# Optimization experiments

Measured on AMD Instinct MI355X. Metric: run time of the kernel, lower is better.

Reference implementation:

```python
import jax, jax.numpy as jnp
import numpy as np

EPS = 1e-8  # torch cosine_similarity default eps


def setup_inputs() -> dict:
    key = jax.random.key(0)
    x = jax.random.normal(key, (256, 200, 1024), dtype=jnp.float32)
    return {"x": x}


def reference(x):
    # x: [B, c, l]
    # Cosine-similarity Gram matrix, fused: dot(i,j) / max(||x_i||*||x_j||, eps)
    norms = jnp.linalg.norm(x, axis=-1)                      # [B, c]
    dots = jnp.einsum('bil,bjl->bij', x, x)                  # [B, c, c]
    sim = dots / jnp.maximum(norms[:, :, None] * norms[:, None, :], EPS)
    atten = jax.nn.softmax(sim, axis=-1)                     # [B, c, c]
    out = jnp.einsum('bij,bjl->bil', atten, x) + x           # bmm + residual
    return out
```

## Files before the change

### kernel.cpp

```cpp
#include <hip/hip_runtime.h>
#include <math.h>


typedef unsigned int uint32;
typedef __attribute__((ext_vector_type(8))) short bf16x8;
typedef __attribute__((ext_vector_type(4))) float f32x4;

#define CC 200
#define LL 1024
#define EPSV 1e-8f
#define PLSTR 116
#define XASTR 36
#define TSTR 116

__device__ __forceinline__ uint32 bfb(float f) {
  uint32 u = __float_as_uint(f);
  u += 0x7fffu + ((u >> 16) & 1u);
  return u >> 16;
}

__global__ __launch_bounds__(512, 1)
void spe_attn_kernel(const float* __restrict__ x, float* __restrict__ out) {
  const int tid  = threadIdx.x;
  const int lane = tid & 63;
  const int w    = tid >> 6;
  const int lm   = lane & 15;
  const int lg   = lane >> 4;
  const int bidx = blockIdx.x;
  const float* xb = x + (size_t)bidx * (CC * LL);
  float* ob       = out + (size_t)bidx * (CC * LL);

  __shared__ uint32 LDS[39312];
  uint32* pl    = LDS;
  uint32* xa0   = LDS + 24128;
  uint32* xa1   = LDS + 31616;
  uint32* xbf0  = LDS + 24128;
  uint32* xbf1  = LDS + 31616;
  float*  norms = (float*)(LDS + 39104);

  const bool two = (w < 5);
  const int rb0 = w;
  const int rb1 = two ? (w + 8) : w;

  const f32x4 fz = {0.f, 0.f, 0.f, 0.f};
  f32x4 acc[2][13];
  #pragma unroll
  for (int i = 0; i < 2; ++i)
    #pragma unroll
    for (int j = 0; j < 13; ++j) acc[i][j] = fz;

  if (tid < 288) { xa0[7200 + tid] = 0u; xa1[7200 + tid] = 0u; }

  float4 vst[7];
  #pragma unroll
  for (int i = 0; i < 7; ++i) {
    int idx = tid + i * 512;
    if (idx < 3200) {
      int row = idx >> 4, c4 = idx & 15;
      vst[i] = *(const float4*)(xb + row * LL + c4 * 4);
    }
  }
  #pragma unroll
  for (int i = 0; i < 7; ++i) {
    int idx = tid + i * 512;
    if (idx < 3200) {
      int row = idx >> 4, c4 = idx & 15;
      uint2 wv;
      wv.x = bfb(vst[i].x) | (bfb(vst[i].y) << 16);
      wv.y = bfb(vst[i].z) | (bfb(vst[i].w) << 16);
      *(uint2*)&xa0[row * XASTR + c4 * 2] = wv;
    }
  }

  for (int s = 0; s < 16; ++s) {
    __syncthreads();
    if (s + 1 < 16) {
      #pragma unroll
      for (int i = 0; i < 7; ++i) {
        int idx = tid + i * 512;
        if (idx < 3200) {
          int row = idx >> 4, c4 = idx & 15;
          vst[i] = *(const float4*)(xb + row * LL + (s + 1) * 64 + c4 * 4);
        }
      }
    }
    const uint32* cur = (s & 1) ? xa1 : xa0;
    __builtin_amdgcn_s_setprio(1);
    #pragma unroll
    for (int ks = 0; ks < 2; ++ks) {
      bf16x8 a0 = *(const bf16x8*)&cur[(rb0 * 16 + lm) * XASTR + ks * 16 + lg * 4];
      bf16x8 a1 = a0;
      if (two) a1 = *(const bf16x8*)&cur[(rb1 * 16 + lm) * XASTR + ks * 16 + lg * 4];
      #pragma unroll
      for (int ct = 0; ct < 13; ++ct) {
        bf16x8 bf = *(const bf16x8*)&cur[(ct * 16 + lm) * XASTR + ks * 16 + lg * 4];
        acc[0][ct] = __builtin_amdgcn_mfma_f32_16x16x32_bf16(a0, bf, acc[0][ct], 0, 0, 0);
        if (two)
          acc[1][ct] = __builtin_amdgcn_mfma_f32_16x16x32_bf16(a1, bf, acc[1][ct], 0, 0, 0);
      }
    }
    __builtin_amdgcn_s_setprio(0);
    if (s + 1 < 16) {
      uint32* nxt = (s & 1) ? xa0 : xa1;
      #pragma unroll
      for (int i = 0; i < 7; ++i) {
        int idx = tid + i * 512;
        if (idx < 3200) {
          int row = idx >> 4, c4 = idx & 15;
          uint2 wv;
          wv.x = bfb(vst[i].x) | (bfb(vst[i].y) << 16);
          wv.y = bfb(vst[i].z) | (bfb(vst[i].w) << 16);
          *(uint2*)&nxt[row * XASTR + c4 * 2] = wv;
        }
      }
    }
  }

  #pragma unroll
  for (int rbi = 0; rbi < 2; ++rbi) {
    if (rbi == 0 || two) {
      int rb = rbi ? rb1 : rb0;
      #pragma unroll
      for (int ct = 0; ct < 13; ++ct) {
        if (ct == rb) {
          #pragma unroll
          for (int r = 0; r < 4; ++r) {
            int ri = lg * 4 + r;
            if (lm == ri) norms[rb * 16 + ri] = sqrtf(acc[rbi][ct][r]);
          }
        }
      }
    }
  }
  __syncthreads();

  float cn[13];
  #pragma unroll
  for (int ct = 0; ct < 13; ++ct) cn[ct] = norms[ct * 16 + lm];

  #pragma unroll
  for (int rbi = 0; rbi < 2; ++rbi) {
    if (rbi == 0 || two) {
      int rb = rbi ? rb1 : rb0;
      #pragma unroll
      for (int r = 0; r < 4; ++r) {
        int grow = rb * 16 + lg * 4 + r;
        float rn = norms[grow];
        float sv[13];
        float m = -INFINITY;
        #pragma unroll
        for (int ct = 0; ct < 13; ++ct) {
          int gc = ct * 16 + lm;
          float sval = acc[rbi][ct][r] / fmaxf(rn * cn[ct], EPSV);
          sval = (gc < CC) ? sval : -INFINITY;
          sv[ct] = sval;
          m = fmaxf(m, sval);
        }
        #pragma unroll
        for (int off = 1; off < 16; off <<= 1) m = fmaxf(m, __shfl_xor(m, off));
        float sum = 0.f;
        #pragma unroll
        for (int ct = 0; ct < 13; ++ct) {
          float e = __expf(sv[ct] - m);
          sv[ct] = e;
          sum += e;
        }
        #pragma unroll
        for (int off = 1; off < 16; off <<= 1) sum += __shfl_xor(sum, off);
        float inv = 1.0f / sum;
        #pragma unroll
        for (int ct = 0; ct < 13; ++ct) {
          int gc = ct * 16 + lm;
          float p = sv[ct] * inv + ((gc == grow) ? 1.0f : 0.0f);
          uint32 pb = bfb(p);
          uint32 qb = (uint32)__shfl_xor((int)pb, 1);
          if (!(lane & 1)) pl[grow * PLSTR + ct * 8 + (lm >> 1)] = pb | (qb << 16);
        }
      }
      for (int i = lane; i < 256; i += 64) {
        int rr = i >> 4, c = i & 15;
        if (c < 12) pl[(rb * 16 + rr) * PLSTR + 100 + c] = 0u;
      }
    }
  }

  bf16x8 pa[2][7];
  #pragma unroll
  for (int ks = 0; ks < 7; ++ks) {
    pa[0][ks] = *(const bf16x8*)&pl[(rb0 * 16 + lm) * PLSTR + ks * 16 + lg * 4];
    if (two)
      pa[1][ks] = *(const bf16x8*)&pl[(rb1 * 16 + lm) * PLSTR + ks * 16 + lg * 4];
  }

  float pv[7][4];
  const int swz = ((lane >> 3) & 3) << 1;
  #pragma unroll
  for (int p = 0; p < 7; ++p) {
    int rb4 = (p * 8 + w) * 4;
    #pragma unroll
    for (int q = 0; q < 4; ++q) {
      int r = rb4 + q;
      pv[p][q] = (r < CC) ? xb[r * LL + lane] : 0.f;
    }
  }
  #pragma unroll
  for (int p = 0; p < 7; ++p) {
    int kpp = p * 8 + w;
    uint2 wv;
    wv.x = bfb(pv[p][0]) | (bfb(pv[p][1]) << 16);
    wv.y = bfb(pv[p][2]) | (bfb(pv[p][3]) << 16);
    *(uint2*)&xbf0[lane * TSTR + 2 * (kpp ^ swz)] = wv;
  }

  for (int nc = 0; nc < 16; ++nc) {
    const int n0 = nc * 64;
    __syncthreads();
    if (nc + 1 < 16) {
      const int n1 = n0 + 64;
      #pragma unroll
      for (int p = 0; p < 7; ++p) {
        int rb4 = (p * 8 + w) * 4;
        #pragma unroll
        for (int q = 0; q < 4; ++q) {
          int r = rb4 + q;
          pv[p][q] = (r < CC) ? xb[r * LL + n1 + lane] : 0.f;
        }
      }
    }

    const uint32* XC = (nc & 1) ? xbf1 : xbf0;
    f32x4 acc2[2][4];
    #pragma unroll
    for (int i = 0; i < 2; ++i)
      #pragma unroll
      for (int j = 0; j < 4; ++j) acc2[i][j] = fz;

    __builtin_amdgcn_s_setprio(1);
    #pragma unroll
    for (int ks = 0; ks < 7; ++ks) {
      #pragma unroll
      for (int ct = 0; ct < 4; ++ct) {
        int col = ct * 16 + lm;
        int s2 = ((col >> 3) & 3) << 1;
        bf16x8 b = *(const bf16x8*)&XC[col * TSTR + 2 * ((ks * 8 + lg * 2) ^ s2)];
        acc2[0][ct] = __builtin_amdgcn_mfma_f32_16x16x32_bf16(pa[0][ks], b, acc2[0][ct], 0, 0, 0);
        if (two)
          acc2[1][ct] = __builtin_amdgcn_mfma_f32_16x16x32_bf16(pa[1][ks], b, acc2[1][ct], 0, 0, 0);
      }
    }
    __builtin_amdgcn_s_setprio(0);

    if (nc + 1 < 16) {
      uint32* XN = (nc & 1) ? xbf0 : xbf1;
      #pragma unroll
      for (int p = 0; p < 7; ++p) {
        int kpp = p * 8 + w;
        uint2 wv;
        wv.x = bfb(pv[p][0]) | (bfb(pv[p][1]) << 16);
        wv.y = bfb(pv[p][2]) | (bfb(pv[p][3]) << 16);
        *(uint2*)&XN[lane * TSTR + 2 * (kpp ^ swz)] = wv;
      }
    }

    #pragma unroll
    for (int rbi = 0; rbi < 2; ++rbi) {
      if (rbi == 0 || two) {
        int rb = rbi ? rb1 : rb0;
        #pragma unroll
        for (int ct = 0; ct < 4; ++ct) {
          #pragma unroll
          for (int r = 0; r < 4; ++r) {
            int grow = rb * 16 + lg * 4 + r;
            if (grow < CC) ob[grow * LL + n0 + ct * 16 + lm] = acc2[rbi][ct][r];
          }
        }
      }
    }
  }
}

extern "C" void kernel_launch(void* const* d_in, const int* in_sizes, int n_in,
                              void* d_out, int out_size, void* d_ws, size_t ws_size,
                              hipStream_t stream) {
  const float* x = (const float*)d_in[0];
  float* out = (float*)d_out;
  const int B = in_sizes[0] / (CC * LL);
  spe_attn_kernel<<<dim3(B), dim3(512), 0, stream>>>(x, out);
}
```

Before: 151.4 us.

## Deepen global-load prefetch to two stages and use lgkm-only barriers

Both GEMM phases now keep two register stages of global loads in flight (loading chunk s+2/s+3 while computing chunk s), instead of one. The phase-2 initial loads are issued before the softmax so their latency overlaps that work. __syncthreads is replaced by a barrier that waits only on LDS counters, so outstanding global loads do not stall the barrier. This roughly doubles the prefetch register footprint, which at 512 threads and one block per CU risks spills.

```diff
diff --git a/kernel.cpp b/kernel.cpp
--- a/kernel.cpp
+++ b/kernel.cpp
@@ -18,6 +18,60 @@
   u += 0x7fffu + ((u >> 16) & 1u);
   return u >> 16;
 }
+
+__device__ __forceinline__ void barrier_lds() {
+  asm volatile("s_waitcnt lgkmcnt(0)" ::: "memory");
+  __builtin_amdgcn_s_barrier();
+  asm volatile("" ::: "memory");
+}
+
+#define P1_LOAD(dst, s_) do {                                              \
+    _Pragma("unroll")                                                      \
+    for (int i = 0; i < 7; ++i) {                                          \
+      int idx = tid + i * 512;                                             \
+      if (idx < 3200) {                                                    \
+        int row = idx >> 4, c4 = idx & 15;                                 \
+        dst[i] = *(const float4*)(xb + row * LL + (s_) * 64 + c4 * 4);     \
+      }                                                                    \
+    }                                                                      \
+  } while (0)
+
+#define P1_WRITE(buf_, src) do {                                           \
+    _Pragma("unroll")                                                      \
+    for (int i = 0; i < 7; ++i) {                                          \
+      int idx = tid + i * 512;                                             \
+      if (idx < 3200) {                                                    \
+        int row = idx >> 4, c4 = idx & 15;                                 \
+        uint2 wv_;                                                         \
+        wv_.x = bfb(src[i].x) | (bfb(src[i].y) << 16);                     \
+        wv_.y = bfb(src[i].z) | (bfb(src[i].w) << 16);                     \
+        *(uint2*)&(buf_)[row * XASTR + c4 * 2] = wv_;                      \
+      }                                                                    \
+    }                                                                      \
+  } while (0)
+
+#define P2_LOAD(dst, n_) do {                                              \
+    _Pragma("unroll")                                                      \
+    for (int p = 0; p < 7; ++p) {                                          \
+      int rb4 = (p * 8 + w) * 4;                                           \
+      _Pragma("unroll")                                                    \
+      for (int q = 0; q < 4; ++q) {                                        \
+        int r = rb4 + q;                                                   \
+        dst[p][q] = (r < CC) ? xb[r * LL + (n_) + lane] : 0.f;             \
+      }                                                                    \
+    }                                                                      \
+  } while (0)
+
+#define P2_WRITE(buf_, src) do {                                           \
+    _Pragma("unroll")                                                      \
+    for (int p = 0; p < 7; ++p) {                                          \
+      int kpp = p * 8 + w;                                                 \
+      uint2 wv_;                                                           \
+      wv_.x = bfb(src[p][0]) | (bfb(src[p][1]) << 16);                     \
+      wv_.y = bfb(src[p][2]) | (bfb(src[p][3]) << 16);                     \
+      *(uint2*)&(buf_)[lane * TSTR + 2 * (kpp ^ swz)] = wv_;               \
+    }                                                                      \
+  } while (0)
 
 __global__ __launch_bounds__(512, 1)
 void spe_attn_kernel(const float* __restrict__ x, float* __restrict__ out) {
@@ -51,39 +105,14 @@
 
   if (tid < 288) { xa0[7200 + tid] = 0u; xa1[7200 + tid] = 0u; }
 
-  float4 vst[7];
-  #pragma unroll
-  for (int i = 0; i < 7; ++i) {
-    int idx = tid + i * 512;
-    if (idx < 3200) {
-      int row = idx >> 4, c4 = idx & 15;
-      vst[i] = *(const float4*)(xb + row * LL + c4 * 4);
-    }
-  }
-  #pragma unroll
-  for (int i = 0; i < 7; ++i) {
-    int idx = tid + i * 512;
-    if (idx < 3200) {
-      int row = idx >> 4, c4 = idx & 15;
-      uint2 wv;
-      wv.x = bfb(vst[i].x) | (bfb(vst[i].y) << 16);
-      wv.y = bfb(vst[i].z) | (bfb(vst[i].w) << 16);
-      *(uint2*)&xa0[row * XASTR + c4 * 2] = wv;
-    }
-  }
+  float4 vstA[7], vstB[7];
+  P1_LOAD(vstA, 0);
+  P1_LOAD(vstB, 1);
+  P1_WRITE(xa0, vstA);
+  P1_LOAD(vstA, 2);
 
   for (int s = 0; s < 16; ++s) {
-    __syncthreads();
-    if (s + 1 < 16) {
-      #pragma unroll
-      for (int i = 0; i < 7; ++i) {
-        int idx = tid + i * 512;
-        if (idx < 3200) {
-          int row = idx >> 4, c4 = idx & 15;
-          vst[i] = *(const float4*)(xb + row * LL + (s + 1) * 64 + c4 * 4);
-        }
-      }
-    }
+    barrier_lds();
     const uint32* cur = (s & 1) ? xa1 : xa0;
     __builtin_amdgcn_s_setprio(1);
     #pragma unroll
@@ -102,19 +131,17 @@
     __builtin_amdgcn_s_setprio(0);
     if (s + 1 < 16) {
       uint32* nxt = (s & 1) ? xa0 : xa1;
-      #pragma unroll
-      for (int i = 0; i < 7; ++i) {
-        int idx = tid + i * 512;
-        if (idx < 3200) {
-          int row = idx >> 4, c4 = idx & 15;
-          uint2 wv;
-          wv.x = bfb(vst[i].x) | (bfb(vst[i].y) << 16);
-          wv.y = bfb(vst[i].z) | (bfb(vst[i].w) << 16);
-          *(uint2*)&nxt[row * XASTR + c4 * 2] = wv;
-        }
-      }
-    }
-  }
+      if (s & 1) { P1_WRITE(nxt, vstA); } else { P1_WRITE(nxt, vstB); }
+    }
+    if (s + 3 < 16) {
+      if (s & 1) { P1_LOAD(vstA, s + 3); } else { P1_LOAD(vstB, s + 3); }
+    }
+  }
+
+  float pv0[7][4], pv1[7][4];
+  const int swz = ((lane >> 3) & 3) << 1;
+  P2_LOAD(pv0, 0);
+  P2_LOAD(pv1, 64);
 
   #pragma unroll
   for (int rbi = 0; rbi < 2; ++rbi) {
@@ -132,7 +159,7 @@
       }
     }
   }
-  __syncthreads();
+  barrier_lds();
 
   float cn[13];
   #pragma unroll
@@ -184,6 +211,9 @@
     }
   }
 
+  P2_WRITE(xbf0, pv0);
+  P2_LOAD(pv0, 128);
+
   bf16x8 pa[2][7];
   #pragma unroll
   for (int ks = 0; ks < 7; ++ks) {
@@ -192,41 +222,9 @@
       pa[1][ks] = *(const bf16x8*)&pl[(rb1 * 16 + lm) * PLSTR + ks * 16 + lg * 4];
   }
 
-  float pv[7][4];
-  const int swz = ((lane >> 3) & 3) << 1;
-  #pragma unroll
-  for (int p = 0; p < 7; ++p) {
-    int rb4 = (p * 8 + w) * 4;
-    #pragma unroll
-    for (int q = 0; q < 4; ++q) {
-      int r = rb4 + q;
-      pv[p][q] = (r < CC) ? xb[r * LL + lane] : 0.f;
-    }
-  }
-  #pragma unroll
-  for (int p = 0; p < 7; ++p) {
-    int kpp = p * 8 + w;
-    uint2 wv;
-    wv.x = bfb(pv[p][0]) | (bfb(pv[p][1]) << 16);
-    wv.y = bfb(pv[p][2]) | (bfb(pv[p][3]) << 16);
-    *(uint2*)&xbf0[lane * TSTR + 2 * (kpp ^ swz)] = wv;
-  }
-
   for (int nc = 0; nc < 16; ++nc) {
     const int n0 = nc * 64;
-    __syncthreads();
-    if (nc + 1 < 16) {
-      const int n1 = n0 + 64;
-      #pragma unroll
-      for (int p = 0; p < 7; ++p) {
-        int rb4 = (p * 8 + w) * 4;
-        #pragma unroll
-        for (int q = 0; q < 4; ++q) {
-          int r = rb4 + q;
-          pv[p][q] = (r < CC) ? xb[r * LL + n1 + lane] : 0.f;
-        }
-      }
-    }
+    barrier_lds();
 
     const uint32* XC = (nc & 1) ? xbf1 : xbf0;
     f32x4 acc2[2][4];
@@ -252,14 +250,10 @@
 
     if (nc + 1 < 16) {
       uint32* XN = (nc & 1) ? xbf0 : xbf1;
-      #pragma unroll
-      for (int p = 0; p < 7; ++p) {
-        int kpp = p * 8 + w;
-        uint2 wv;
-        wv.x = bfb(pv[p][0]) | (bfb(pv[p][1]) << 16);
-        wv.y = bfb(pv[p][2]) | (bfb(pv[p][3]) << 16);
-        *(uint2*)&XN[lane * TSTR + 2 * (kpp ^ swz)] = wv;
-      }
+      if (nc & 1) { P2_WRITE(XN, pv0); } else { P2_WRITE(XN, pv1); }
+    }
+    if (nc + 3 < 16) {
+      if (nc & 1) { P2_LOAD(pv0, (nc + 3) * 64); } else { P2_LOAD(pv1, (nc + 3) * 64); }
     }
 
     #pragma unroll
```

Result: slower. 343.0 us (+126.5%).
